# Kernel tuning notes

Hardware: AMD Instinct MI355X
Metric: run time of the kernel (lower is better)

## Reference

```python
import jax, jax.numpy as jnp
import numpy as np
import math

SCALE = 32.0
M_BASE = 0.5
ALPHA = 0.1
BETA = 0.15
HARD_RATIO = 0.2
NUM_CLASSES = 100000
EMB = 512
B = 256
SIN_M = math.sin(M_BASE)


def setup_inputs() -> dict:
    key = jax.random.key(0)
    k1, k2, k3 = jax.random.split(key, 3)
    features = jax.random.normal(k1, (B, EMB), dtype=jnp.float32)
    labels = jax.random.randint(k2, (B,), 0, NUM_CLASSES, dtype=jnp.int64)
    # xavier_uniform for (num_classes, embedding_size)
    limit = math.sqrt(6.0 / (NUM_CLASSES + EMB))
    kernel = jax.random.uniform(k3, (NUM_CLASSES, EMB), dtype=jnp.float32,
                                minval=-limit, maxval=limit)
    return {"features": features, "labels": labels, "kernel": kernel}


def _l2norm(x, axis=1, eps=1e-12):
    n = jnp.sqrt(jnp.sum(x * x, axis=axis, keepdims=True))
    return x / jnp.maximum(n, eps)


def reference(features, labels, kernel):
    f = _l2norm(features)                     # (B, E)
    w = _l2norm(kernel)                       # (C, E)
    cos_theta = jnp.clip(f @ w.T, -1.0, 1.0)  # (B, C)

    rows = jnp.arange(cos_theta.shape[0])
    cos_y = cos_theta[rows, labels][:, None]          # (B, 1)
    difficulty = 1.0 - jax.lax.stop_gradient(cos_y)   # (B, 1), detached
    hard_threshold = jnp.quantile(difficulty, HARD_RATIO)
    hard_mask = (difficulty >= hard_threshold).astype(cos_theta.dtype)
    m = M_BASE + ALPHA * difficulty + BETA * hard_mask  # (B, 1)

    # non-easy-margin branch of the original module
    cos_theta_m = cos_theta - m * SIN_M - (1.0 - jnp.cos(m * jnp.pi)) * cos_theta

    one_hot_y = (labels[:, None] == jnp.arange(cos_theta.shape[1])[None, :])
    output = jnp.where(one_hot_y, cos_theta_m, cos_theta) * SCALE

    # cross entropy
    logp = jax.nn.log_softmax(output, axis=1)
    loss = -jnp.mean(logp[rows, labels])
    return loss
```

## Files before the change

kernel.cpp:

```cpp
#include <hip/hip_runtime.h>

typedef __bf16 bf16x8 __attribute__((ext_vector_type(8)));
typedef __bf16 bf16x4 __attribute__((ext_vector_type(4)));
typedef float  f32x4  __attribute__((ext_vector_type(4)));

#define EMB 512
#define NROWS 256
#define BN 64
#define NCOPY 16
#define K_SCALE_LOG2E 46.16624130844683f
#define SIN_M_ 0.479425538604203f
#define PI_ 3.14159265358979323846f

__device__ __forceinline__ unsigned short f2bf(float f) {
    union { float f; unsigned u; } x; x.f = f;
    return (unsigned short)((x.u + 0x7FFFu + ((x.u >> 16) & 1u)) >> 16);
}

__device__ __forceinline__ int swz(int logical) {
    return logical ^ ((((logical >> 10) & 7) ^ ((logical >> 8) & 3)) << 4);
}

__global__ void prep_kernel(const float* __restrict__ F, const int* __restrict__ labels,
                            const float* __restrict__ W,
                            unsigned short* __restrict__ Abf,
                            float* __restrict__ cos_y, float* __restrict__ expsum) {
    const int row = blockIdx.x, t = threadIdx.x;
    const int lbl = labels[row];
    float2 fv = reinterpret_cast<const float2*>(F + (size_t)row * EMB)[t];
    float2 wv = reinterpret_cast<const float2*>(W + (size_t)lbl * EMB)[t];
    float ff = fv.x * fv.x + fv.y * fv.y;
    float fw = fv.x * wv.x + fv.y * wv.y;
    float ww = wv.x * wv.x + wv.y * wv.y;
    #pragma unroll
    for (int m = 1; m < 64; m <<= 1) {
        ff += __shfl_xor(ff, m); fw += __shfl_xor(fw, m); ww += __shfl_xor(ww, m);
    }
    __shared__ float sf[4], sb[4], sc[4];
    if ((t & 63) == 0) { int w = t >> 6; sf[w] = ff; sb[w] = fw; sc[w] = ww; }
    __syncthreads();
    const float a = sf[0] + sf[1] + sf[2] + sf[3];
    const float inv = 1.f / fmaxf(sqrtf(a), 1e-12f);
    ushort2 o; o.x = f2bf(fv.x * inv); o.y = f2bf(fv.y * inv);
    reinterpret_cast<ushort2*>(Abf + (size_t)row * EMB)[t] = o;
    if (t < NCOPY) expsum[t * NROWS + row] = 0.f;
    if (t == 0) {
        const float b = sb[0] + sb[1] + sb[2] + sb[3];
        const float c = sc[0] + sc[1] + sc[2] + sc[3];
        const float cs = b / (fmaxf(sqrtf(a), 1e-12f) * fmaxf(sqrtf(c), 1e-12f));
        cos_y[row] = fminf(fmaxf(cs, -1.f), 1.f);
    }
}

__global__ __launch_bounds__(512, 4) void gemm_lse(
    const unsigned short* __restrict__ A,
    const float* __restrict__ W,
    float* __restrict__ expsum,
    int C) {
    __shared__ unsigned short sW[BN * EMB];
    __shared__ float s_invw[BN];

    const int t = threadIdx.x;
    const int chunk = blockIdx.x;
    const int cls_l = t >> 3;
    const int slice = t & 7;
    const int cls_g = chunk * BN + cls_l;
    const bool valid = (cls_g < C);
    char* sWc = reinterpret_cast<char*>(sW);

    const float4* src = reinterpret_cast<const float4*>(
        W + (size_t)(valid ? cls_g : 0) * EMB);
    float ss = 0.f;
    #pragma unroll 8
    for (int i = 0; i < 16; ++i) {
        float4 v = src[i * 8 + slice];
        if (!valid) { v.x = 0.f; v.y = 0.f; v.z = 0.f; v.w = 0.f; }
        ss += v.x * v.x + v.y * v.y + v.z * v.z + v.w * v.w;
        bf16x4 p;
        p.x = (__bf16)v.x; p.y = (__bf16)v.y; p.z = (__bf16)v.z; p.w = (__bf16)v.w;
        const int logical = cls_l * (EMB * 2) + i * 64 + slice * 8;
        *reinterpret_cast<bf16x4*>(sWc + swz(logical)) = p;
    }
    ss += __shfl_xor(ss, 1);
    ss += __shfl_xor(ss, 2);
    ss += __shfl_xor(ss, 4);
    if (slice == 0) s_invw[cls_l] = valid ? 1.f / fmaxf(sqrtf(ss), 1e-12f) : 0.f;
    __syncthreads();

    const int wave = t >> 6;
    const int lane = t & 63;
    const int g = lane >> 4;
    const int r16 = lane & 15;

    f32x4 acc[2][4];
    #pragma unroll
    for (int mb = 0; mb < 2; ++mb)
        #pragma unroll
        for (int nb = 0; nb < 4; ++nb) acc[mb][nb] = f32x4{0.f, 0.f, 0.f, 0.f};

    #pragma unroll 4
    for (int kk = 0; kk < EMB / 32; ++kk) {
        bf16x8 bfr[4], afr[2];
        #pragma unroll
        for (int nb = 0; nb < 4; ++nb) {
            const int logical = (nb * 16 + r16) * (EMB * 2) + kk * 64 + g * 16;
            bfr[nb] = *reinterpret_cast<const bf16x8*>(sWc + swz(logical));
        }
        #pragma unroll
        for (int mb = 0; mb < 2; ++mb) {
            const int row = wave * 32 + mb * 16 + r16;
            afr[mb] = *reinterpret_cast<const bf16x8*>(A + (size_t)row * EMB + kk * 32 + g * 8);
        }
        #pragma unroll
        for (int mb = 0; mb < 2; ++mb)
            #pragma unroll
            for (int nb = 0; nb < 4; ++nb)
                acc[mb][nb] = __builtin_amdgcn_mfma_f32_16x16x32_bf16(
                    afr[mb], bfr[nb], acc[mb][nb], 0, 0, 0);
    }

    float* dst = expsum + (chunk & (NCOPY - 1)) * NROWS;
    float iw[4], msk[4];
    #pragma unroll
    for (int nb = 0; nb < 4; ++nb) {
        iw[nb] = s_invw[nb * 16 + r16];
        msk[nb] = ((chunk * BN + nb * 16 + r16) < C) ? 1.f : 0.f;
    }
    #pragma unroll
    for (int mb = 0; mb < 2; ++mb) {
        #pragma unroll
        for (int r = 0; r < 4; ++r) {
            float rs = 0.f;
            #pragma unroll
            for (int nb = 0; nb < 4; ++nb) {
                float cs = acc[mb][nb][r] * iw[nb];
                cs = fminf(fmaxf(cs, -1.f), 1.f);
                rs += msk[nb] * exp2f(cs * K_SCALE_LOG2E - K_SCALE_LOG2E);
            }
            rs += __shfl_xor(rs, 1);
            rs += __shfl_xor(rs, 2);
            rs += __shfl_xor(rs, 4);
            rs += __shfl_xor(rs, 8);
            if (r16 == 0) atomicAdd(&dst[wave * 32 + mb * 16 + g * 4 + r], rs);
        }
    }
}

__global__ void finish_kernel(const float* __restrict__ cos_y,
                              const float* __restrict__ expsum,
                              float* __restrict__ out) {
    __shared__ float sd[NROWS];
    __shared__ float s_thr;
    __shared__ float s[4];
    const int i = threadIdx.x;
    const float cy = cos_y[i];
    const float d = 1.f - cy;
    sd[i] = d;
    __syncthreads();
    int lt = 0, eq = 0;
    for (int j = 0; j < NROWS; ++j) {
        const float dj = sd[j];
        lt += (dj < d); eq += (dj == d);
    }
    if (lt <= 51 && 51 < lt + eq) s_thr = d;
    __syncthreads();
    const float hard = (d >= s_thr) ? 1.f : 0.f;
    const float m = 0.5f + 0.1f * d + 0.15f * hard;
    const float cosm = cy - m * SIN_M_ - (1.f - cosf(m * PI_)) * cy;
    const float sub = exp2f(cy   * K_SCALE_LOG2E - K_SCALE_LOG2E);
    const float add = exp2f(cosm * K_SCALE_LOG2E - K_SCALE_LOG2E);
    float S = 0.f;
    #pragma unroll
    for (int c = 0; c < NCOPY; ++c) S += expsum[c * NROWS + i];
    S += add - sub;
    float term = 32.f + logf(S) - 32.f * cosm;
    #pragma unroll
    for (int mm = 1; mm < 64; mm <<= 1) term += __shfl_xor(term, mm);
    if ((i & 63) == 0) s[i >> 6] = term;
    __syncthreads();
    if (i == 0) out[0] = (s[0] + s[1] + s[2] + s[3]) * (1.f / 256.f);
}

extern "C" void kernel_launch(void* const* d_in, const int* in_sizes, int n_in,
                              void* d_out, int out_size, void* d_ws, size_t ws_size,
                              hipStream_t stream) {
    (void)n_in; (void)out_size; (void)ws_size;
    const float* F      = (const float*)d_in[0];
    const int*   labels = (const int*)d_in[1];
    const float* W      = (const float*)d_in[2];
    float* out = (float*)d_out;
    const int C = in_sizes[2] / EMB;

    char* ws = (char*)d_ws;
    unsigned short* Abf = (unsigned short*)ws;
    float* cos_y  = (float*)(ws + 262144);
    float* expsum = cos_y + NROWS;

    const int nchunk = (C + BN - 1) / BN;

    hipLaunchKernelGGL(prep_kernel,   dim3(NROWS),  dim3(256), 0, stream,
                       F, labels, W, Abf, cos_y, expsum);
    hipLaunchKernelGGL(gemm_lse,      dim3(nchunk), dim3(512), 0, stream, Abf, W, expsum, C);
    hipLaunchKernelGGL(finish_kernel, dim3(1),      dim3(256), 0, stream,
                       cos_y, expsum, out);
}
```

Before: 330.8 us.

## Make GEMM-LSE kernel persistent with double-buffered weight prefetch

```diff
diff --git a/kernel.cpp b/kernel.cpp
--- a/kernel.cpp
+++ b/kernel.cpp
@@ -6,7 +6,8 @@
 
 #define EMB 512
 #define NROWS 256
-#define BN 64
+#define BNC 32
+#define NBLK 512
 #define NCOPY 16
 #define K_SCALE_LOG2E 46.16624130844683f
 #define SIN_M_ 0.479425538604203f
@@ -57,86 +58,145 @@
     const float* __restrict__ W,
     float* __restrict__ expsum,
     int C) {
-    __shared__ unsigned short sW[BN * EMB];
-    __shared__ float s_invw[BN];
+    __shared__ unsigned short sW[2][BNC * EMB];
+    __shared__ float s_invw[2][BNC];
 
     const int t = threadIdx.x;
-    const int chunk = blockIdx.x;
-    const int cls_l = t >> 3;
-    const int slice = t & 7;
-    const int cls_g = chunk * BN + cls_l;
-    const bool valid = (cls_g < C);
-    char* sWc = reinterpret_cast<char*>(sW);
-
-    const float4* src = reinterpret_cast<const float4*>(
-        W + (size_t)(valid ? cls_g : 0) * EMB);
-    float ss = 0.f;
-    #pragma unroll 8
-    for (int i = 0; i < 16; ++i) {
-        float4 v = src[i * 8 + slice];
-        if (!valid) { v.x = 0.f; v.y = 0.f; v.z = 0.f; v.w = 0.f; }
-        ss += v.x * v.x + v.y * v.y + v.z * v.z + v.w * v.w;
-        bf16x4 p;
-        p.x = (__bf16)v.x; p.y = (__bf16)v.y; p.z = (__bf16)v.z; p.w = (__bf16)v.w;
-        const int logical = cls_l * (EMB * 2) + i * 64 + slice * 8;
-        *reinterpret_cast<bf16x4*>(sWc + swz(logical)) = p;
-    }
-    ss += __shfl_xor(ss, 1);
-    ss += __shfl_xor(ss, 2);
-    ss += __shfl_xor(ss, 4);
-    if (slice == 0) s_invw[cls_l] = valid ? 1.f / fmaxf(sqrtf(ss), 1e-12f) : 0.f;
-    __syncthreads();
-
+    const int bid = blockIdx.x;
+    const int nchunk = (C + BNC - 1) / BNC;
+    const int cls_l = t >> 4;
+    const int slice = t & 15;
     const int wave = t >> 6;
     const int lane = t & 63;
     const int g = lane >> 4;
     const int r16 = lane & 15;
 
-    f32x4 acc[2][4];
+    float rsacc[2][4];
     #pragma unroll
     for (int mb = 0; mb < 2; ++mb)
         #pragma unroll
-        for (int nb = 0; nb < 4; ++nb) acc[mb][nb] = f32x4{0.f, 0.f, 0.f, 0.f};
-
-    #pragma unroll 4
-    for (int kk = 0; kk < EMB / 32; ++kk) {
-        bf16x8 bfr[4], afr[2];
-        #pragma unroll
-        for (int nb = 0; nb < 4; ++nb) {
-            const int logical = (nb * 16 + r16) * (EMB * 2) + kk * 64 + g * 16;
-            bfr[nb] = *reinterpret_cast<const bf16x8*>(sWc + swz(logical));
-        }
-        #pragma unroll
-        for (int mb = 0; mb < 2; ++mb) {
-            const int row = wave * 32 + mb * 16 + r16;
-            afr[mb] = *reinterpret_cast<const bf16x8*>(A + (size_t)row * EMB + kk * 32 + g * 8);
-        }
+        for (int r = 0; r < 4; ++r) rsacc[mb][r] = 0.f;
+
+    char* sb0 = reinterpret_cast<char*>(&sW[0][0]);
+    char* sb1 = reinterpret_cast<char*>(&sW[1][0]);
+
+    int c = bid;
+    float4 vr[8];
+    if (c < nchunk) {
+        const int cg = c * BNC + cls_l;
+        const bool v = (cg < C);
+        const float4* src = reinterpret_cast<const float4*>(
+            W + (size_t)(v ? cg : 0) * EMB);
+        #pragma unroll
+        for (int i = 0; i < 8; ++i) vr[i] = src[i * 16 + slice];
+        float ss = 0.f;
+        #pragma unroll
+        for (int i = 0; i < 8; ++i) {
+            float4 x = vr[i];
+            if (!v) { x.x = 0.f; x.y = 0.f; x.z = 0.f; x.w = 0.f; }
+            ss += x.x * x.x + x.y * x.y + x.z * x.z + x.w * x.w;
+            bf16x4 p;
+            p.x = (__bf16)x.x; p.y = (__bf16)x.y; p.z = (__bf16)x.z; p.w = (__bf16)x.w;
+            *reinterpret_cast<bf16x4*>(sb0 + swz(cls_l * 1024 + i * 128 + slice * 8)) = p;
+        }
+        ss += __shfl_xor(ss, 1);
+        ss += __shfl_xor(ss, 2);
+        ss += __shfl_xor(ss, 4);
+        ss += __shfl_xor(ss, 8);
+        if (slice == 0) s_invw[0][cls_l] = v ? 1.f / fmaxf(sqrtf(ss), 1e-12f) : 0.f;
+    }
+    __syncthreads();
+
+    int cur = 0;
+    while (c < nchunk) {
+        const int nc = c + NBLK;
+        const bool hn = (nc < nchunk);
+
+        bool v2 = false;
+        if (hn) {
+            const int cg = nc * BNC + cls_l;
+            v2 = (cg < C);
+            const float4* src = reinterpret_cast<const float4*>(
+                W + (size_t)(v2 ? cg : 0) * EMB);
+            #pragma unroll
+            for (int i = 0; i < 8; ++i) vr[i] = src[i * 16 + slice];
+        }
+
+        const char* sb = cur ? sb1 : sb0;
+        f32x4 acc[2][2];
         #pragma unroll
         for (int mb = 0; mb < 2; ++mb)
             #pragma unroll
-            for (int nb = 0; nb < 4; ++nb)
-                acc[mb][nb] = __builtin_amdgcn_mfma_f32_16x16x32_bf16(
-                    afr[mb], bfr[nb], acc[mb][nb], 0, 0, 0);
-    }
-
-    float* dst = expsum + (chunk & (NCOPY - 1)) * NROWS;
-    float iw[4], msk[4];
-    #pragma unroll
-    for (int nb = 0; nb < 4; ++nb) {
-        iw[nb] = s_invw[nb * 16 + r16];
-        msk[nb] = ((chunk * BN + nb * 16 + r16) < C) ? 1.f : 0.f;
-    }
+            for (int nb = 0; nb < 2; ++nb) acc[mb][nb] = f32x4{0.f, 0.f, 0.f, 0.f};
+
+        #pragma unroll 4
+        for (int kk = 0; kk < EMB / 32; ++kk) {
+            bf16x8 bfr[2], afr[2];
+            #pragma unroll
+            for (int nb = 0; nb < 2; ++nb) {
+                const int logical = (nb * 16 + r16) * 1024 + kk * 64 + g * 16;
+                bfr[nb] = *reinterpret_cast<const bf16x8*>(sb + swz(logical));
+            }
+            #pragma unroll
+            for (int mb = 0; mb < 2; ++mb) {
+                const int row = wave * 32 + mb * 16 + r16;
+                afr[mb] = *reinterpret_cast<const bf16x8*>(
+                    A + (size_t)row * EMB + kk * 32 + g * 8);
+            }
+            #pragma unroll
+            for (int mb = 0; mb < 2; ++mb)
+                #pragma unroll
+                for (int nb = 0; nb < 2; ++nb)
+                    acc[mb][nb] = __builtin_amdgcn_mfma_f32_16x16x32_bf16(
+                        afr[mb], bfr[nb], acc[mb][nb], 0, 0, 0);
+        }
+
+        {
+            const float iw0 = s_invw[cur][r16];
+            const float iw1 = s_invw[cur][16 + r16];
+            const float m0 = ((c * BNC + r16) < C) ? 1.f : 0.f;
+            const float m1 = ((c * BNC + 16 + r16) < C) ? 1.f : 0.f;
+            #pragma unroll
+            for (int mb = 0; mb < 2; ++mb) {
+                #pragma unroll
+                for (int r = 0; r < 4; ++r) {
+                    float cs0 = fminf(fmaxf(acc[mb][0][r] * iw0, -1.f), 1.f);
+                    float cs1 = fminf(fmaxf(acc[mb][1][r] * iw1, -1.f), 1.f);
+                    rsacc[mb][r] += m0 * exp2f(cs0 * K_SCALE_LOG2E - K_SCALE_LOG2E)
+                                  + m1 * exp2f(cs1 * K_SCALE_LOG2E - K_SCALE_LOG2E);
+                }
+            }
+        }
+
+        if (hn) {
+            char* sbn = cur ? sb0 : sb1;
+            float ss = 0.f;
+            #pragma unroll
+            for (int i = 0; i < 8; ++i) {
+                float4 x = vr[i];
+                if (!v2) { x.x = 0.f; x.y = 0.f; x.z = 0.f; x.w = 0.f; }
+                ss += x.x * x.x + x.y * x.y + x.z * x.z + x.w * x.w;
+                bf16x4 p;
+                p.x = (__bf16)x.x; p.y = (__bf16)x.y; p.z = (__bf16)x.z; p.w = (__bf16)x.w;
+                *reinterpret_cast<bf16x4*>(sbn + swz(cls_l * 1024 + i * 128 + slice * 8)) = p;
+            }
+            ss += __shfl_xor(ss, 1);
+            ss += __shfl_xor(ss, 2);
+            ss += __shfl_xor(ss, 4);
+            ss += __shfl_xor(ss, 8);
+            if (slice == 0) s_invw[cur ^ 1][cls_l] = v2 ? 1.f / fmaxf(sqrtf(ss), 1e-12f) : 0.f;
+        }
+        __syncthreads();
+        cur ^= 1;
+        c = nc;
+    }
+
+    float* dst = expsum + (bid & (NCOPY - 1)) * NROWS;
     #pragma unroll
     for (int mb = 0; mb < 2; ++mb) {
         #pragma unroll
         for (int r = 0; r < 4; ++r) {
-            float rs = 0.f;
-            #pragma unroll
-            for (int nb = 0; nb < 4; ++nb) {
-                float cs = acc[mb][nb][r] * iw[nb];
-                cs = fminf(fmaxf(cs, -1.f), 1.f);
-                rs += msk[nb] * exp2f(cs * K_SCALE_LOG2E - K_SCALE_LOG2E);
-            }
+            float rs = rsacc[mb][r];
             rs += __shfl_xor(rs, 1);
             rs += __shfl_xor(rs, 2);
             rs += __shfl_xor(rs, 4);
@@ -171,7 +231,7 @@
     const float add = exp2f(cosm * K_SCALE_LOG2E - K_SCALE_LOG2E);
     float S = 0.f;
     #pragma unroll
-    for (int c = 0; c < NCOPY; ++c) S += expsum[c * NROWS + i];
+    for (int cc = 0; cc < NCOPY; ++cc) S += expsum[cc * NROWS + i];
     S += add - sub;
     float term = 32.f + logf(S) - 32.f * cosm;
     #pragma unroll
@@ -196,11 +256,9 @@
     float* cos_y  = (float*)(ws + 262144);
     float* expsum = cos_y + NROWS;
 
-    const int nchunk = (C + BN - 1) / BN;
-
-    hipLaunchKernelGGL(prep_kernel,   dim3(NROWS),  dim3(256), 0, stream,
+    hipLaunchKernelGGL(prep_kernel,   dim3(NROWS), dim3(256), 0, stream,
                        F, labels, W, Abf, cos_y, expsum);
-    hipLaunchKernelGGL(gemm_lse,      dim3(nchunk), dim3(512), 0, stream, Abf, W, expsum, C);
-    hipLaunchKernelGGL(finish_kernel, dim3(1),      dim3(256), 0, stream,
+    hipLaunchKernelGGL(gemm_lse,      dim3(NBLK),  dim3(512), 0, stream, Abf, W, expsum, C);
+    hipLaunchKernelGGL(finish_kernel, dim3(1),     dim3(256), 0, stream,
                        cos_y, expsum, out);
 }
```

After: 352.0 us. 1.06x slower.

## Persistent grid with multi-buffered async global-to-LDS weight staging

Applied to the files above, without the earlier changes.

```diff
diff --git a/kernel.cpp b/kernel.cpp
--- a/kernel.cpp
+++ b/kernel.cpp
@@ -1,12 +1,13 @@
 #include <hip/hip_runtime.h>
 
 typedef __bf16 bf16x8 __attribute__((ext_vector_type(8)));
-typedef __bf16 bf16x4 __attribute__((ext_vector_type(4)));
 typedef float  f32x4  __attribute__((ext_vector_type(4)));
 
 #define EMB 512
 #define NROWS 256
-#define BN 64
+#define BNC 16
+#define GRID 256
+#define NBUF 4
 #define NCOPY 16
 #define K_SCALE_LOG2E 46.16624130844683f
 #define SIN_M_ 0.479425538604203f
@@ -15,10 +16,6 @@
 __device__ __forceinline__ unsigned short f2bf(float f) {
     union { float f; unsigned u; } x; x.f = f;
     return (unsigned short)((x.u + 0x7FFFu + ((x.u >> 16) & 1u)) >> 16);
-}
-
-__device__ __forceinline__ int swz(int logical) {
-    return logical ^ ((((logical >> 10) & 7) ^ ((logical >> 8) & 3)) << 4);
 }
 
 __global__ void prep_kernel(const float* __restrict__ F, const int* __restrict__ labels,
@@ -52,96 +49,141 @@
     }
 }
 
-__global__ __launch_bounds__(512, 4) void gemm_lse(
+__device__ __forceinline__ void stage_chunk(const float* __restrict__ W, int C, int chunk,
+                                            char* buf, int wave, int lane) {
+    #pragma unroll
+    for (int it = 0; it < 4; ++it) {
+        const int wi = wave * 4 + it;
+        const int c  = wi >> 1;
+        const int h  = wi & 1;
+        int cg = chunk * BNC + c;
+        if (cg >= C) cg = 0;
+        const float* gp = W + (size_t)cg * EMB + h * 256 + ((lane ^ (c & 7)) << 2);
+        __builtin_amdgcn_global_load_lds(
+            (const __attribute__((address_space(1))) void*)gp,
+            (__attribute__((address_space(3))) void*)(buf + wi * 1024),
+            16, 0, 0);
+    }
+}
+
+__global__ __launch_bounds__(512, 2) void gemm_lse(
     const unsigned short* __restrict__ A,
     const float* __restrict__ W,
     float* __restrict__ expsum,
     int C) {
-    __shared__ unsigned short sW[BN * EMB];
-    __shared__ float s_invw[BN];
+    __shared__ float sW[NBUF * BNC * EMB];
+    __shared__ float s_invw[BNC];
 
     const int t = threadIdx.x;
-    const int chunk = blockIdx.x;
-    const int cls_l = t >> 3;
-    const int slice = t & 7;
-    const int cls_g = chunk * BN + cls_l;
-    const bool valid = (cls_g < C);
-    char* sWc = reinterpret_cast<char*>(sW);
-
-    const float4* src = reinterpret_cast<const float4*>(
-        W + (size_t)(valid ? cls_g : 0) * EMB);
-    float ss = 0.f;
-    #pragma unroll 8
-    for (int i = 0; i < 16; ++i) {
-        float4 v = src[i * 8 + slice];
-        if (!valid) { v.x = 0.f; v.y = 0.f; v.z = 0.f; v.w = 0.f; }
-        ss += v.x * v.x + v.y * v.y + v.z * v.z + v.w * v.w;
-        bf16x4 p;
-        p.x = (__bf16)v.x; p.y = (__bf16)v.y; p.z = (__bf16)v.z; p.w = (__bf16)v.w;
-        const int logical = cls_l * (EMB * 2) + i * 64 + slice * 8;
-        *reinterpret_cast<bf16x4*>(sWc + swz(logical)) = p;
-    }
-    ss += __shfl_xor(ss, 1);
-    ss += __shfl_xor(ss, 2);
-    ss += __shfl_xor(ss, 4);
-    if (slice == 0) s_invw[cls_l] = valid ? 1.f / fmaxf(sqrtf(ss), 1e-12f) : 0.f;
-    __syncthreads();
-
+    const int bid = blockIdx.x;
     const int wave = t >> 6;
     const int lane = t & 63;
     const int g = lane >> 4;
     const int r16 = lane & 15;
-
-    f32x4 acc[2][4];
-    #pragma unroll
-    for (int mb = 0; mb < 2; ++mb)
+    const int NCH = (C + BNC - 1) / BNC;
+    char* sWc = reinterpret_cast<char*>(sW);
+
+    bf16x8 afr0[16], afr1[16];
+    {
+        const unsigned short* a0 = A + (size_t)(wave * 32 + r16) * EMB + g * 8;
+        const unsigned short* a1 = A + (size_t)(wave * 32 + 16 + r16) * EMB + g * 8;
         #pragma unroll
-        for (int nb = 0; nb < 4; ++nb) acc[mb][nb] = f32x4{0.f, 0.f, 0.f, 0.f};
-
-    #pragma unroll 4
-    for (int kk = 0; kk < EMB / 32; ++kk) {
-        bf16x8 bfr[4], afr[2];
+        for (int kk = 0; kk < 16; ++kk) {
+            afr0[kk] = *reinterpret_cast<const bf16x8*>(a0 + kk * 32);
+            afr1[kk] = *reinterpret_cast<const bf16x8*>(a1 + kk * 32);
+        }
+    }
+
+    float rs0[4] = {0.f, 0.f, 0.f, 0.f};
+    float rs1[4] = {0.f, 0.f, 0.f, 0.f};
+
+    int j  = bid;
+    int jp = bid;
+    #pragma unroll
+    for (int d = 0; d < NBUF - 1; ++d) {
+        if (jp < NCH) {
+            stage_chunk(W, C, jp, sWc + (((jp - bid) >> 8) & (NBUF - 1)) * 32768, wave, lane);
+            jp += GRID;
+        }
+    }
+
+    while (j < NCH) {
+        const int inflight = (jp - j) >> 8;
+        if (inflight >= 3)      asm volatile("s_waitcnt vmcnt(8) lgkmcnt(0)" ::: "memory");
+        else if (inflight == 2) asm volatile("s_waitcnt vmcnt(4) lgkmcnt(0)" ::: "memory");
+        else                    asm volatile("s_waitcnt vmcnt(0) lgkmcnt(0)" ::: "memory");
+        __builtin_amdgcn_s_barrier();
+        __builtin_amdgcn_sched_barrier(0);
+
+        char* buf = sWc + (((j - bid) >> 8) & (NBUF - 1)) * 32768;
+
+        if (jp < NCH) {
+            stage_chunk(W, C, jp, sWc + (((jp - bid) >> 8) & (NBUF - 1)) * 32768, wave, lane);
+            jp += GRID;
+        }
+
+        {
+            const int c0 = wave * 2 + (lane >> 5);
+            const int li = lane & 31;
+            const char* tb = buf + c0 * 2048;
+            const int mr = (c0 & 7) << 4;
+            float ssum = 0.f;
+            #pragma unroll
+            for (int s = 0; s < 4; ++s) {
+                float4 v = *reinterpret_cast<const float4*>(tb + ((s * 512 + li * 16) ^ mr));
+                ssum += v.x * v.x + v.y * v.y + v.z * v.z + v.w * v.w;
+            }
+            ssum += __shfl_xor(ssum, 1);
+            ssum += __shfl_xor(ssum, 2);
+            ssum += __shfl_xor(ssum, 4);
+            ssum += __shfl_xor(ssum, 8);
+            ssum += __shfl_xor(ssum, 16);
+            if (li == 0) s_invw[c0] = 1.f / fmaxf(sqrtf(ssum), 1e-12f);
+        }
+        asm volatile("s_waitcnt lgkmcnt(0)" ::: "memory");
+        __builtin_amdgcn_s_barrier();
+        __builtin_amdgcn_sched_barrier(0);
+
+        f32x4 acc0 = {0.f, 0.f, 0.f, 0.f};
+        f32x4 acc1 = {0.f, 0.f, 0.f, 0.f};
+        const char* bb = buf + r16 * 2048;
+        const int off0 = (g << 5) ^ ((r16 & 7) << 4);
         #pragma unroll
-        for (int nb = 0; nb < 4; ++nb) {
-            const int logical = (nb * 16 + r16) * (EMB * 2) + kk * 64 + g * 16;
-            bfr[nb] = *reinterpret_cast<const bf16x8*>(sWc + swz(logical));
-        }
-        #pragma unroll
-        for (int mb = 0; mb < 2; ++mb) {
-            const int row = wave * 32 + mb * 16 + r16;
-            afr[mb] = *reinterpret_cast<const bf16x8*>(A + (size_t)row * EMB + kk * 32 + g * 8);
-        }
-        #pragma unroll
-        for (int mb = 0; mb < 2; ++mb)
+        for (int kk = 0; kk < 16; ++kk) {
+            float4 lo = *reinterpret_cast<const float4*>(bb + kk * 128 + off0);
+            float4 hi = *reinterpret_cast<const float4*>(bb + kk * 128 + (off0 ^ 16));
+            bf16x8 bf;
+            bf[0] = (__bf16)lo.x; bf[1] = (__bf16)lo.y; bf[2] = (__bf16)lo.z; bf[3] = (__bf16)lo.w;
+            bf[4] = (__bf16)hi.x; bf[5] = (__bf16)hi.y; bf[6] = (__bf16)hi.z; bf[7] = (__bf16)hi.w;
+            acc0 = __builtin_amdgcn_mfma_f32_16x16x32_bf16(afr0[kk], bf, acc0, 0, 0, 0);
+            acc1 = __builtin_amdgcn_mfma_f32_16x16x32_bf16(afr1[kk], bf, acc1, 0, 0, 0);
+        }
+
+        {
+            const float iw = s_invw[r16];
+            const float mk = ((j * BNC + r16) < C) ? 1.f : 0.f;
             #pragma unroll
-            for (int nb = 0; nb < 4; ++nb)
-                acc[mb][nb] = __builtin_amdgcn_mfma_f32_16x16x32_bf16(
-                    afr[mb], bfr[nb], acc[mb][nb], 0, 0, 0);
-    }
-
-    float* dst = expsum + (chunk & (NCOPY - 1)) * NROWS;
-    float iw[4], msk[4];
-    #pragma unroll
-    for (int nb = 0; nb < 4; ++nb) {
-        iw[nb] = s_invw[nb * 16 + r16];
-        msk[nb] = ((chunk * BN + nb * 16 + r16) < C) ? 1.f : 0.f;
-    }
-    #pragma unroll
-    for (int mb = 0; mb < 2; ++mb) {
-        #pragma unroll
-        for (int r = 0; r < 4; ++r) {
-            float rs = 0.f;
-            #pragma unroll
-            for (int nb = 0; nb < 4; ++nb) {
-                float cs = acc[mb][nb][r] * iw[nb];
-                cs = fminf(fmaxf(cs, -1.f), 1.f);
-                rs += msk[nb] * exp2f(cs * K_SCALE_LOG2E - K_SCALE_LOG2E);
+            for (int r = 0; r < 4; ++r) {
+                float c0v = fminf(fmaxf(acc0[r] * iw, -1.f), 1.f);
+                float c1v = fminf(fmaxf(acc1[r] * iw, -1.f), 1.f);
+                rs0[r] += mk * exp2f(c0v * K_SCALE_LOG2E - K_SCALE_LOG2E);
+                rs1[r] += mk * exp2f(c1v * K_SCALE_LOG2E - K_SCALE_LOG2E);
             }
-            rs += __shfl_xor(rs, 1);
-            rs += __shfl_xor(rs, 2);
-            rs += __shfl_xor(rs, 4);
-            rs += __shfl_xor(rs, 8);
-            if (r16 == 0) atomicAdd(&dst[wave * 32 + mb * 16 + g * 4 + r], rs);
+        }
+        j += GRID;
+    }
+
+    float* dst = expsum + (bid & (NCOPY - 1)) * NROWS;
+    #pragma unroll
+    for (int r = 0; r < 4; ++r) {
+        float a0v = rs0[r], a1v = rs1[r];
+        a0v += __shfl_xor(a0v, 1); a0v += __shfl_xor(a0v, 2);
+        a0v += __shfl_xor(a0v, 4); a0v += __shfl_xor(a0v, 8);
+        a1v += __shfl_xor(a1v, 1); a1v += __shfl_xor(a1v, 2);
+        a1v += __shfl_xor(a1v, 4); a1v += __shfl_xor(a1v, 8);
+        if (r16 == 0) {
+            atomicAdd(&dst[wave * 32 + g * 4 + r], a0v);
+            atomicAdd(&dst[wave * 32 + 16 + g * 4 + r], a1v);
         }
     }
 }
@@ -158,8 +200,8 @@
     sd[i] = d;
     __syncthreads();
     int lt = 0, eq = 0;
-    for (int j = 0; j < NROWS; ++j) {
-        const float dj = sd[j];
+    for (int jj = 0; jj < NROWS; ++jj) {
+        const float dj = sd[jj];
         lt += (dj < d); eq += (dj == d);
     }
     if (lt <= 51 && 51 < lt + eq) s_thr = d;
@@ -171,7 +213,7 @@
     const float add = exp2f(cosm * K_SCALE_LOG2E - K_SCALE_LOG2E);
     float S = 0.f;
     #pragma unroll
-    for (int c = 0; c < NCOPY; ++c) S += expsum[c * NROWS + i];
+    for (int cc = 0; cc < NCOPY; ++cc) S += expsum[cc * NROWS + i];
     S += add - sub;
     float term = 32.f + logf(S) - 32.f * cosm;
     #pragma unroll
@@ -196,11 +238,9 @@
     float* cos_y  = (float*)(ws + 262144);
     float* expsum = cos_y + NROWS;
 
-    const int nchunk = (C + BN - 1) / BN;
-
-    hipLaunchKernelGGL(prep_kernel,   dim3(NROWS),  dim3(256), 0, stream,
+    hipLaunchKernelGGL(prep_kernel,   dim3(NROWS), dim3(256), 0, stream,
                        F, labels, W, Abf, cos_y, expsum);
-    hipLaunchKernelGGL(gemm_lse,      dim3(nchunk), dim3(512), 0, stream, Abf, W, expsum, C);
-    hipLaunchKernelGGL(finish_kernel, dim3(1),      dim3(256), 0, stream,
+    hipLaunchKernelGGL(gemm_lse,      dim3(GRID),  dim3(512), 0, stream, Abf, W, expsum, C);
+    hipLaunchKernelGGL(finish_kernel, dim3(1),     dim3(256), 0, stream,
                        cos_y, expsum, out);
 }
```

After: 298.3 us. 1.11x faster.
